# Kernel tuning notes

Measured on AMD Instinct MI355X. Metric: run time of the kernel, lower is better.

The kernel has to match this reference:

```python
import jax, jax.numpy as jnp
import numpy as np

B = 8          # events per batch
NPB = 8192     # points per event (equal counts -> Nmax = NPB)
N = B * NPB
FEAT = 6
K = 128        # max_tokens
TOK = 768      # token_dim
KNN = 16       # k_neighbors
MLP_DIMS = [FEAT, 256, 512, 768, TOK]


def setup_inputs() -> dict:
    key = jax.random.key(0)
    ks = jax.random.split(key, 20)
    coords = jax.random.normal(ks[0], (N, 3), jnp.float32) * 5.0
    features = jax.random.normal(ks[1], (N, FEAT), jnp.float32)
    times = jax.random.uniform(ks[2], (N, 1), jnp.float32)
    # equal-sized, sorted batch ids (8192 points per event)
    batch_ids = jnp.repeat(jnp.arange(B, dtype=jnp.int32), NPB)
    inp = {"coords": coords, "features": features, "batch_ids": batch_ids, "times": times}
    # per-point MLP: 6 -> 256 -> 512 -> 768 -> 768 (last Linear has no ReLU)
    ki = 3
    for i in range(4):
        din, dout = MLP_DIMS[i], MLP_DIMS[i + 1]
        inp[f"W{i+1}"] = jax.random.normal(ks[ki], (din, dout), jnp.float32) / np.sqrt(din); ki += 1
        inp[f"b{i+1}"] = jnp.zeros((dout,), jnp.float32)
    # neighborhood MLP: 768 -> 768 -> 768
    inp["Wn1"] = jax.random.normal(ks[ki], (TOK, TOK), jnp.float32) / np.sqrt(TOK); ki += 1
    inp["bn1"] = jnp.zeros((TOK,), jnp.float32)
    inp["Wn2"] = jax.random.normal(ks[ki], (TOK, TOK), jnp.float32) / np.sqrt(TOK); ki += 1
    inp["bn2"] = jnp.zeros((TOK,), jnp.float32)
    return inp


def _forward(coords, features, batch_ids, times,
             W1, b1, W2, b2, W3, b3, W4, b4, Wn1, bn1, Wn2, bn2):
    INF = jnp.float32(jnp.inf)
    points4 = jnp.concatenate([coords[:, :3], times], axis=-1)  # [N,4] (x,y,z,t)
    # per-point MLP
    h = jax.nn.relu(features @ W1 + b1)
    h = jax.nn.relu(h @ W2 + b2)
    h = jax.nn.relu(h @ W3 + b3)
    feats = h @ W4 + b4                                          # [N,TOK]
    # ---- pack flat -> padded [B, NPB, *] ----
    counts = jnp.bincount(batch_ids, length=B)                   # [B]
    offsets = jnp.cumsum(counts) - counts
    pos = jnp.arange(N) - offsets[batch_ids]
    P = jnp.zeros((B, NPB, 4), points4.dtype).at[batch_ids, pos].set(points4)
    Fp = jnp.zeros((B, NPB, TOK), feats.dtype).at[batch_ids, pos].set(feats)
    valid = jnp.arange(NPB)[None, :] < counts[:, None]           # [B,NPB]
    # ---- small path: take first K points sorted by time ----
    tsort = jnp.where(valid, P[..., 3], INF)
    sorted_idx = jnp.argsort(tsort, axis=1)[:, :K]               # K <= NPB
    tokens_small = jnp.take_along_axis(Fp, sorted_idx[..., None], axis=1)
    cents_small = jnp.take_along_axis(P, sorted_idx[..., None], axis=1)
    masks_small = jnp.arange(K)[None, :] < jnp.minimum(counts, K)[:, None]
    tokens_small = tokens_small * masks_small[..., None]
    cents_small = cents_small * masks_small[..., None]
    # ---- batched FPS over 4D points ----
    min_d0 = jnp.where(valid, INF, 0.0)
    norms = jnp.where(valid, jnp.sum(P * P, axis=-1), -INF)
    first = jnp.argmax(norms, axis=1)                            # farthest-from-origin start
    barange = jnp.arange(B)
    def fps_step(carry, _):
        min_d, last = carry
        c = P[barange, last]                                     # [B,4]
        d = jnp.sum((P - c[:, None, :]) ** 2, axis=-1)
        d = jnp.where(valid, d, INF)
        min_d = jnp.minimum(min_d, d)
        return (min_d, jnp.argmax(min_d, axis=1)), last
    _, idx_seq = jax.lax.scan(fps_step, (min_d0, first), None, length=K)
    fps_idx = idx_seq.T                                          # [B,K]
    validK = jnp.arange(K)[None, :] < jnp.minimum(counts, K)[:, None]
    cents_large = jnp.take_along_axis(P, fps_idx[..., None], axis=1)  # [B,K,4]
    # ---- kNN pooling around centroids ----
    diff = cents_large[:, :, None, :] - P[:, None, :, :]         # [B,K,NPB,4]
    dists = jnp.sum(diff * diff, axis=-1)                        # [B,K,NPB]
    dists = jnp.where(valid[:, None, :], dists, INF)
    k_g = min(KNN, NPB)
    _, knn_idx = jax.lax.top_k(-dists, k_g)                      # smallest-k -> [B,K,k]
    knn_valid = jnp.take_along_axis(jnp.broadcast_to(valid[:, None, :], (B, K, NPB)), knn_idx, axis=2)
    neigh = jnp.take_along_axis(Fp[:, None, :, :], knn_idx[..., None], axis=2)  # [B,K,k,TOK]
    masked = jnp.where(knn_valid[..., None], neigh, -INF)
    pooled = jnp.max(masked, axis=2)
    pooled = jnp.where(jnp.isfinite(pooled), pooled, 0.0)
    tokens_large = jax.nn.relu(pooled @ Wn1 + bn1) @ Wn2 + bn2   # [B,K,TOK]
    # sort selected tokens by centroid time
    ctimes = jnp.where(validK, cents_large[..., 3], INF)
    order = jnp.argsort(ctimes, axis=1)
    tokens_large = jnp.take_along_axis(tokens_large, order[..., None], axis=1)
    cents_large = jnp.take_along_axis(cents_large, order[..., None], axis=1)
    masks_large = jnp.take_along_axis(validK, order, axis=1)
    tokens_large = tokens_large * masks_large[..., None]
    cents_large = cents_large * masks_large[..., None]
    # ---- select per-event path ----
    small = counts <= K
    tokens = jnp.where(small[:, None, None], tokens_small, tokens_large)
    cents = jnp.where(small[:, None, None], cents_small, cents_large)
    masks = jnp.where(small[:, None], masks_small, masks_large)
    return tokens, cents, masks


def reference(coords, features, batch_ids, times,
              W1, b1, W2, b2, W3, b3, W4, b4, Wn1, bn1, Wn2, bn2):
    return _forward(coords, features, batch_ids, times,
                    W1, b1, W2, b2, W3, b3, W4, b4, Wn1, bn1, Wn2, bn2)
```

## Files before the change

kernel.cpp:

```cpp
#include <hip/hip_runtime.h>
#include <hip/hip_bf16.h>


#define BEV 8
#define NPB 8192
#define FEAT 6
#define KTOK 128
#define TOK 768
#define KNN 16

typedef unsigned short ushort_t;
typedef unsigned long long u64;
typedef __bf16 bf16x8 __attribute__((ext_vector_type(8)));
typedef float f32x4 __attribute__((ext_vector_type(4)));
typedef float f32x2 __attribute__((ext_vector_type(2)));

__device__ __forceinline__ ushort_t f2b(float f) {
    union { float f; unsigned int i; } x; x.f = f;
    unsigned int i = x.i;
    unsigned int r = (i + 0x7FFFu + ((i >> 16) & 1u)) >> 16;
    return (ushort_t)r;
}

#define DPP_ROW_SHR1  0x111
#define DPP_ROW_SHR2  0x112
#define DPP_ROW_SHR4  0x114
#define DPP_ROW_SHR8  0x118
#define DPP_ROW_BC15  0x142
#define DPP_ROW_BC31  0x143

template <int CTRL>
__device__ __forceinline__ float dpp_fmax(float v) {
    int o = __builtin_amdgcn_update_dpp(__float_as_int(v), __float_as_int(v),
                                        CTRL, 0xf, 0xf, false);
    return fmaxf(v, __int_as_float(o));
}

template <int CTRL>
__device__ __forceinline__ u64 dpp_u64max(u64 k) {
    int lo = (int)(unsigned)(k & 0xFFFFFFFFu);
    int hi = (int)(unsigned)(k >> 32);
    unsigned olo = (unsigned)__builtin_amdgcn_update_dpp(lo, lo, CTRL, 0xf, 0xf, false);
    unsigned ohi = (unsigned)__builtin_amdgcn_update_dpp(hi, hi, CTRL, 0xf, 0xf, false);
    u64 o = ((u64)ohi << 32) | (u64)olo;
    return o > k ? o : k;
}

__global__ __launch_bounds__(256) void fill_kernel(float* __restrict__ out, int n) {
    int i = blockIdx.x * 256 + threadIdx.x;
    if (i < n) out[i] = 0.f;
}

__global__ __launch_bounds__(1024) void fps_kernel(
    const float* __restrict__ coords, const float* __restrict__ times,
    float* __restrict__ cents, int* __restrict__ pos,
    float* __restrict__ cents_out, float* __restrict__ masks_out)
{
#pragma clang fp contract(off)
    const int b = blockIdx.x;
    const int t = threadIdx.x;
    __shared__ u64   slotk[2][16];
    __shared__ float tarr[KTOK];
    __shared__ float carr[KTOK][4];
    f32x2 px[4], py[4], pz[4], pw[4], md[4];
    const long base = (long)b * NPB;
#pragma unroll
    for (int i = 0; i < 4; ++i) {
        long g = base + t * 8 + i * 2;
        px[i] = (f32x2){coords[g * 3 + 0], coords[(g + 1) * 3 + 0]};
        py[i] = (f32x2){coords[g * 3 + 1], coords[(g + 1) * 3 + 1]};
        pz[i] = (f32x2){coords[g * 3 + 2], coords[(g + 1) * 3 + 2]};
        pw[i] = (f32x2){times[g], times[g + 1]};
        md[i] = (f32x2){__builtin_inff(), __builtin_inff()};
    }
    const int wv = t >> 6, lane = t & 63;
    float cx = 0.f, cy = 0.f, cz = 0.f, cw = 0.f;
    for (int s = 0; s < KTOK; ++s) {
        f32x2 v[4];
        if (s == 0) {
#pragma unroll
            for (int i = 0; i < 4; ++i)
                v[i] = ((px[i]*px[i] + py[i]*py[i]) + pz[i]*pz[i]) + pw[i]*pw[i];
        } else {
            const f32x2 c2x = {cx, cx}, c2y = {cy, cy}, c2z = {cz, cz}, c2w = {cw, cw};
#pragma unroll
            for (int i = 0; i < 4; ++i) {
                f32x2 dx = px[i] - c2x, dy = py[i] - c2y;
                f32x2 dz = pz[i] - c2z, dw = pw[i] - c2w;
                f32x2 d = ((dx*dx + dy*dy) + dz*dz) + dw*dw;
                md[i] = __builtin_elementwise_min(md[i], d);
                v[i] = md[i];
            }
        }
        f32x2 m01 = __builtin_elementwise_max(v[0], v[1]);
        f32x2 m23 = __builtin_elementwise_max(v[2], v[3]);
        f32x2 mm  = __builtin_elementwise_max(m01, m23);
        const float bv = fmaxf(mm[0], mm[1]);
        float mvv = bv;
        mvv = dpp_fmax<DPP_ROW_SHR1>(mvv);
        mvv = dpp_fmax<DPP_ROW_SHR2>(mvv);
        mvv = dpp_fmax<DPP_ROW_SHR4>(mvv);
        mvv = dpp_fmax<DPP_ROW_SHR8>(mvv);
        mvv = dpp_fmax<DPP_ROW_BC15>(mvv);
        mvv = dpp_fmax<DPP_ROW_BC31>(mvv);
        const float mv = __int_as_float(__builtin_amdgcn_readlane(__float_as_int(mvv), 63));
        const u64 mask = __ballot(bv == mv);
        const int wl = __ffsll((long long)mask) - 1;
        const int p = s & 1;
        if (lane == wl) {
            int bi = t * 8;
#pragma unroll
            for (int j = 7; j >= 0; --j)
                if (v[j >> 1][j & 1] == mv) bi = t * 8 + j;
            slotk[p][wv] = ((u64)__float_as_uint(mv) << 32)
                         | (unsigned)(NPB - 1 - bi);
        }
        __syncthreads();
        u64 k1 = slotk[p][lane & 15];
        k1 = dpp_u64max<DPP_ROW_SHR1>(k1);
        k1 = dpp_u64max<DPP_ROW_SHR2>(k1);
        k1 = dpp_u64max<DPP_ROW_SHR4>(k1);
        k1 = dpp_u64max<DPP_ROW_SHR8>(k1);
        const unsigned klo =
            (unsigned)__builtin_amdgcn_readlane((int)(unsigned)(k1 & 0xFFFFFFFFu), 15);
        const int widx = NPB - 1 - (int)klo;
        const long gc = base + widx;
        cx = coords[gc * 3 + 0]; cy = coords[gc * 3 + 1];
        cz = coords[gc * 3 + 2]; cw = times[gc];
        if (t == 0) {
            tarr[s] = cw;
            carr[s][0] = cx; carr[s][1] = cy; carr[s][2] = cz; carr[s][3] = cw;
        }
    }
    __syncthreads();
    if (t < KTOK) {
        const float ti = tarr[t];
        int rank = 0;
        for (int j = 0; j < KTOK; ++j) {
            float tj = tarr[j];
            if (tj < ti || (tj == ti && j < t)) ++rank;
        }
        rank &= (KTOK - 1);
        pos[b * KTOK + t] = rank;
        float* cc = &cents[(b * KTOK + t) * 4];
        cc[0] = carr[t][0]; cc[1] = carr[t][1];
        cc[2] = carr[t][2]; cc[3] = carr[t][3];
#pragma unroll
        for (int c = 0; c < 4; ++c)
            cents_out[(b * KTOK + rank) * 4 + c] = carr[t][c];
        masks_out[b * KTOK + t] = 1.0f;
    }
}

__global__ __launch_bounds__(256) void knn_tc(
    const float* __restrict__ coords, const float* __restrict__ times,
    const float* __restrict__ cents, int* __restrict__ knn_idx,
    const float* __restrict__ W2, ushort_t* __restrict__ Wt2,
    const float* __restrict__ W3, ushort_t* __restrict__ Wt3,
    const float* __restrict__ W4, ushort_t* __restrict__ Wt4)
{
#pragma clang fp contract(off)
    __shared__ float tile[32][33];
    __shared__ float rv[4];
    __shared__ int   ri[4];
    const int blk = blockIdx.x;
    if (blk >= BEV * KTOK) {
        const int id = blk - BEV * KTOK;
        const float* in; ushort_t* out; int K, N, bx, by;
        if (id < 128)      { in = W2; out = Wt2; K = 256; N = 512;
                             bx = id & 15; by = id >> 4; }
        else if (id < 512) { in = W3; out = Wt3; K = 512; N = 768;
                             int r = id - 128; bx = r % 24; by = r / 24; }
        else               { in = W4; out = Wt4; K = 768; N = 768;
                             int r = id - 512; bx = r % 24; by = r / 24; }
        const int tt = threadIdx.x, tx = tt & 31, ty = tt >> 5;
#pragma unroll
        for (int r = 0; r < 4; ++r) {
            int y = by * 32 + ty + r * 8;
            tile[ty + r * 8][tx] = in[(long)y * N + bx * 32 + tx];
        }
        __syncthreads();
        const int ko = by * 32 + tx;
#pragma unroll
        for (int r = 0; r < 4; ++r) {
            int no = bx * 32 + ty + r * 8;
            out[(long)no * K + ko] = f2b(tile[tx][ty + r * 8]);
        }
        return;
    }
    const int b = blk >> 7;
    const int t = threadIdx.x;
    const float cx = cents[blk*4+0], cy = cents[blk*4+1];
    const float cz = cents[blk*4+2], cw = cents[blk*4+3];
    float d[32];
    const long base = (long)b * NPB;
#pragma unroll
    for (int i = 0; i < 32; ++i) {
        long g = base + t * 32 + i;
        float dx = coords[g*3+0] - cx;
        float dy = coords[g*3+1] - cy;
        float dz = coords[g*3+2] - cz;
        float dw = times[g] - cw;
        d[i] = ((dx*dx + dy*dy) + dz*dz) + dw*dw;
    }
    const int wv = t >> 6, lane = t & 63;
    for (int pass = 0; pass < KNN; ++pass) {
        float bvv = __builtin_inff(); int bii = t * 32;
#pragma unroll
        for (int i = 0; i < 32; ++i)
            if (d[i] < bvv) { bvv = d[i]; bii = t * 32 + i; }
        for (int off = 1; off < 64; off <<= 1) {
            float ov = __shfl_xor(bvv, off);
            int   oi = __shfl_xor(bii, off);
            if (ov < bvv || (ov == bvv && oi < bii)) { bvv = ov; bii = oi; }
        }
        if (lane == 0) { rv[wv] = bvv; ri[wv] = bii; }
        __syncthreads();
        float gb = __builtin_inff(); int winner = 0;
        for (int wI = 0; wI < 4; ++wI) {
            float v = rv[wI]; int idx = ri[wI];
            if (v < gb || (v == gb && idx < winner)) { gb = v; winner = idx; }
        }
        winner &= (NPB - 1);
#pragma unroll
        for (int i = 0; i < 32; ++i)
            if (t * 32 + i == winner) d[i] = __builtin_inff();
        if (t == 0) knn_idx[blk * KNN + pass] = winner;
        __syncthreads();
    }
}

#define PAD1 264
#define PAD2 520
#define PAD3 776
__global__ __launch_bounds__(256, 2) void mlp_fused(
    const float* __restrict__ features, const float* __restrict__ W1,
    const float* __restrict__ b1, const int* __restrict__ knn_idx,
    const ushort_t* __restrict__ Wt2, const float* __restrict__ b2,
    const ushort_t* __restrict__ Wt3, const float* __restrict__ b3,
    const ushort_t* __restrict__ Wt4, const float* __restrict__ b4,
    ushort_t* __restrict__ pooled)
{
    __shared__ __align__(16) ushort_t lds[35904];
    ushort_t* h1 = lds;
    ushort_t* h2 = lds + 8448;
    ushort_t* h3 = lds;
    ushort_t* Bs = lds + 25088;
    float*    feat = (float*)(lds + 35328);
    int*      pidx = (int*)(lds + 35840);

    const int bi = blockIdx.x;
    const int t = threadIdx.x;
    const int w = t >> 6, lane = t & 63;
    const int ln = lane & 15, q = lane >> 4;

    if (t < 32) {
        const int c = bi * 2 + (t >> 4);
        const int ev = c >> 7;
        pidx[t] = ev * NPB + (knn_idx[c * KNN + (t & 15)] & (NPB - 1));
    }
    __syncthreads();
    if (t < 192) {
        const int r = t / 6, f = t - r * 6;
        feat[r * 8 + f] = features[(long)pidx[r] * FEAT + f];
    }
    __syncthreads();
    {
        float wv[FEAT];
#pragma unroll
        for (int f = 0; f < FEAT; ++f) wv[f] = W1[f * 256 + t];
        const float bias = b1[t];
#pragma unroll
        for (int r = 0; r < 32; ++r) {
            float acc = 0.f;
#pragma unroll
            for (int f = 0; f < FEAT; ++f) acc += feat[r * 8 + f] * wv[f];
            h1[r * PAD1 + t] = f2b(fmaxf(acc + bias, 0.f));
        }
    }
    __syncthreads();

    {
        f32x4 acc[2][8];
#pragma unroll
        for (int m = 0; m < 2; ++m)
#pragma unroll
            for (int i = 0; i < 8; ++i) acc[m][i] = (f32x4){0,0,0,0};
        for (int k0 = 0; k0 < 256; k0 += 32) {
            bf16x8 af[2];
#pragma unroll
            for (int m = 0; m < 2; ++m)
                af[m] = *(const bf16x8*)(&h1[(m * 16 + ln) * PAD1 + k0 + q * 8]);
#pragma unroll
            for (int np = 0; np < 2; ++np) {
                __syncthreads();
#pragma unroll
                for (int i = 0; i < 4; ++i) {
                    int e = t + i * 256, n = e >> 2, sk = e & 3;
                    *(uint4*)(&Bs[n * 40 + sk * 8]) =
                        *(const uint4*)(Wt2 + (long)(np * 256 + n) * 256 + k0 + sk * 8);
                }
                __syncthreads();
#pragma unroll
                for (int j = 0; j < 4; ++j) {
                    bf16x8 bf = *(const bf16x8*)(&Bs[((w * 4 + j) * 16 + ln) * 40 + q * 8]);
#pragma unroll
                    for (int m = 0; m < 2; ++m)
                        acc[m][np * 4 + j] = __builtin_amdgcn_mfma_f32_16x16x32_bf16(af[m], bf, acc[m][np * 4 + j], 0, 0, 0);
                }
            }
        }
        __syncthreads();
#pragma unroll
        for (int np = 0; np < 2; ++np)
#pragma unroll
            for (int j = 0; j < 4; ++j) {
                const int col = np * 256 + (w * 4 + j) * 16 + ln;
                const float bias = b2[col];
#pragma unroll
                for (int m = 0; m < 2; ++m)
#pragma unroll
                    for (int r = 0; r < 4; ++r)
                        h2[(m * 16 + q * 4 + r) * PAD2 + col] = f2b(fmaxf(acc[m][np * 4 + j][r] + bias, 0.f));
            }
    }
    __syncthreads();

    {
        f32x4 acc[2][12];
#pragma unroll
        for (int m = 0; m < 2; ++m)
#pragma unroll
            for (int i = 0; i < 12; ++i) acc[m][i] = (f32x4){0,0,0,0};
        for (int k0 = 0; k0 < 512; k0 += 32) {
            bf16x8 af[2];
#pragma unroll
            for (int m = 0; m < 2; ++m)
                af[m] = *(const bf16x8*)(&h2[(m * 16 + ln) * PAD2 + k0 + q * 8]);
#pragma unroll
            for (int np = 0; np < 3; ++np) {
                __syncthreads();
#pragma unroll
                for (int i = 0; i < 4; ++i) {
                    int e = t + i * 256, n = e >> 2, sk = e & 3;
                    *(uint4*)(&Bs[n * 40 + sk * 8]) =
                        *(const uint4*)(Wt3 + (long)(np * 256 + n) * 512 + k0 + sk * 8);
                }
                __syncthreads();
#pragma unroll
                for (int j = 0; j < 4; ++j) {
                    bf16x8 bf = *(const bf16x8*)(&Bs[((w * 4 + j) * 16 + ln) * 40 + q * 8]);
#pragma unroll
                    for (int m = 0; m < 2; ++m)
                        acc[m][np * 4 + j] = __builtin_amdgcn_mfma_f32_16x16x32_bf16(af[m], bf, acc[m][np * 4 + j], 0, 0, 0);
                }
            }
        }
        __syncthreads();
#pragma unroll
        for (int np = 0; np < 3; ++np)
#pragma unroll
            for (int j = 0; j < 4; ++j) {
                const int col = np * 256 + (w * 4 + j) * 16 + ln;
                const float bias = b3[col];
#pragma unroll
                for (int m = 0; m < 2; ++m)
#pragma unroll
                    for (int r = 0; r < 4; ++r)
                        h3[(m * 16 + q * 4 + r) * PAD3 + col] = f2b(fmaxf(acc[m][np * 4 + j][r] + bias, 0.f));
            }
    }
    __syncthreads();

    {
        f32x4 acc[2][12];
#pragma unroll
        for (int m = 0; m < 2; ++m)
#pragma unroll
            for (int i = 0; i < 12; ++i) acc[m][i] = (f32x4){0,0,0,0};
        for (int k0 = 0; k0 < 768; k0 += 32) {
            bf16x8 af[2];
#pragma unroll
            for (int m = 0; m < 2; ++m)
                af[m] = *(const bf16x8*)(&h3[(m * 16 + ln) * PAD3 + k0 + q * 8]);
#pragma unroll
            for (int np = 0; np < 3; ++np) {
                __syncthreads();
#pragma unroll
                for (int i = 0; i < 4; ++i) {
                    int e = t + i * 256, n = e >> 2, sk = e & 3;
                    *(uint4*)(&Bs[n * 40 + sk * 8]) =
                        *(const uint4*)(Wt4 + (long)(np * 256 + n) * 768 + k0 + sk * 8);
                }
                __syncthreads();
#pragma unroll
                for (int j = 0; j < 4; ++j) {
                    bf16x8 bf = *(const bf16x8*)(&Bs[((w * 4 + j) * 16 + ln) * 40 + q * 8]);
#pragma unroll
                    for (int m = 0; m < 2; ++m)
                        acc[m][np * 4 + j] = __builtin_amdgcn_mfma_f32_16x16x32_bf16(af[m], bf, acc[m][np * 4 + j], 0, 0, 0);
                }
            }
        }
#pragma unroll
        for (int np = 0; np < 3; ++np)
#pragma unroll
            for (int j = 0; j < 4; ++j) {
                const int col = np * 256 + (w * 4 + j) * 16 + ln;
#pragma unroll
                for (int m = 0; m < 2; ++m) {
                    float v = fmaxf(fmaxf(acc[m][np * 4 + j][0], acc[m][np * 4 + j][1]),
                                    fmaxf(acc[m][np * 4 + j][2], acc[m][np * 4 + j][3]));
                    v = fmaxf(v, __shfl_xor(v, 16));
                    v = fmaxf(v, __shfl_xor(v, 32));
                    if (q == 0)
                        pooled[(long)(bi * 2 + m) * TOK + col] = f2b(v + b4[col]);
                }
            }
    }
}

template<int EPI, int RELU, int F32OUT>
__global__ __launch_bounds__(256) void gemm64_kn(
    const ushort_t* __restrict__ A, const float* __restrict__ B,
    const float* __restrict__ bias, void* __restrict__ Cv,
    int M, int N, int Kd, const int* __restrict__ pos)
{
    __shared__ __align__(16) ushort_t As[64 * 40];
    __shared__ __align__(16) ushort_t Bsh[64 * 40];
    ushort_t* Cb = (ushort_t*)Cv;
    float*    Cf = (float*)Cv;
    const int tid = threadIdx.x;
    const int m0 = blockIdx.x * 64;
    const int n0 = blockIdx.y * 64;
    const int w = tid >> 6, lane = tid & 63;
    const int ln = lane & 15, q = lane >> 4;
    f32x4 acc[4];
#pragma unroll
    for (int ni = 0; ni < 4; ++ni) acc[ni] = (f32x4){0.f, 0.f, 0.f, 0.f};

    const int ar = tid >> 2, as0 = (tid & 3) * 8;
    const int kk = tid >> 4, nn = (tid & 15) * 4;

    for (int k0 = 0; k0 < Kd; k0 += 32) {
        __syncthreads();
        uint4 a0 = *(const uint4*)(A + (long)(m0 + ar) * Kd + k0 + as0);
        float4 f0 = *(const float4*)(B + (long)(k0 + kk)      * N + n0 + nn);
        float4 f1 = *(const float4*)(B + (long)(k0 + kk + 16) * N + n0 + nn);
        *(uint4*)(&As[ar * 40 + as0]) = a0;
        float e0[4] = {f0.x, f0.y, f0.z, f0.w};
        float e1[4] = {f1.x, f1.y, f1.z, f1.w};
#pragma unroll
        for (int j = 0; j < 4; ++j) Bsh[(nn + j) * 40 + kk]      = f2b(e0[j]);
#pragma unroll
        for (int j = 0; j < 4; ++j) Bsh[(nn + j) * 40 + kk + 16] = f2b(e1[j]);
        __syncthreads();
        bf16x8 af = *(const bf16x8*)(&As[(w * 16 + ln) * 40 + q * 8]);
#pragma unroll
        for (int ni = 0; ni < 4; ++ni) {
            bf16x8 bf = *(const bf16x8*)(&Bsh[(ni * 16 + ln) * 40 + q * 8]);
            acc[ni] = __builtin_amdgcn_mfma_f32_16x16x32_bf16(af, bf, acc[ni], 0, 0, 0);
        }
    }

#pragma unroll
    for (int ni = 0; ni < 4; ++ni) {
        const int col = n0 + ni * 16 + ln;
        const float bv = bias[col];
#pragma unroll
        for (int r = 0; r < 4; ++r) {
            const int row = m0 + w * 16 + q * 4 + r;
            float v = acc[ni][r] + bv;
            if (EPI == 0) {
                if (RELU) v = fmaxf(v, 0.f);
                if (F32OUT) Cf[(long)row * N + col] = v;
                else        Cb[(long)row * N + col] = f2b(v);
            } else {
                const int orow = (row & ~(KTOK - 1)) + (pos[row] & (KTOK - 1));
                if (F32OUT) Cf[(long)orow * N + col] = v;
                else        Cb[(long)orow * N + col] = f2b(v);
            }
        }
    }
}

extern "C" void kernel_launch(void* const* d_in, const int* in_sizes, int n_in,
                              void* d_out, int out_size, void* d_ws, size_t ws_size,
                              hipStream_t stream)
{
    const float* coords   = (const float*)d_in[0];
    const float* features = (const float*)d_in[1];
    const float* times    = (const float*)d_in[3];
    const float* W1  = (const float*)d_in[4];
    const float* b1  = (const float*)d_in[5];
    const float* W2  = (const float*)d_in[6];
    const float* b2  = (const float*)d_in[7];
    const float* W3  = (const float*)d_in[8];
    const float* b3  = (const float*)d_in[9];
    const float* W4  = (const float*)d_in[10];
    const float* b4  = (const float*)d_in[11];
    const float* Wn1 = (const float*)d_in[12];
    const float* bn1 = (const float*)d_in[13];
    const float* Wn2 = (const float*)d_in[14];
    const float* bn2 = (const float*)d_in[15];

    char* ws = (char*)d_ws;
    float*    cents   = (float*)(ws + 0);
    int*      pos     = (int*)(ws + 16384);
    int*      knn_idx = (int*)(ws + 20480);
    ushort_t* t1      = (ushort_t*)(ws + 86016);
    ushort_t* pooled  = (ushort_t*)(ws + 1658880);
    ushort_t* Wt2b    = (ushort_t*)(ws + 3231744);
    ushort_t* Wt3b    = (ushort_t*)(ws + 3493888);
    ushort_t* Wt4b    = (ushort_t*)(ws + 4280320);
    const long WS_NEED = 5459968;

    float* tokens_out = (float*)d_out;
    float* cents_out  = tokens_out + 786432;
    float* masks_out  = tokens_out + 790528;

    if ((long)ws_size < WS_NEED) {
        fill_kernel<<<(791552 + 255) / 256, 256, 0, stream>>>(tokens_out, 791552);
        return;
    }

    fps_kernel<<<BEV, 1024, 0, stream>>>(coords, times, cents, pos,
                                         cents_out, masks_out);

    knn_tc<<<BEV * KTOK + 1088, 256, 0, stream>>>(coords, times, cents, knn_idx,
                                                  W2, Wt2b, W3, Wt3b, W4, Wt4b);

    mlp_fused<<<512, 256, 0, stream>>>(features, W1, b1, knn_idx,
                                       Wt2b, b2, Wt3b, b3, Wt4b, b4, pooled);

    gemm64_kn<0,1,0><<<dim3(16, 12), 256, 0, stream>>>(pooled, Wn1, bn1, t1, 1024, 768, 768, nullptr);
    gemm64_kn<2,0,1><<<dim3(16, 12), 256, 0, stream>>>(t1, Wn2, bn2, tokens_out, 1024, 768, 768, pos);
}
```

Measured before the change: 432.7 us.

## Double rows per block and K-step in fused MLP to halve weight traffic

The fused point MLP kernel now handles 4 centroids (64 rows) per 512-thread block instead of 2 centroids per 256-thread block, with two wave groups sharing each staged weight tile. Each staging step loads a 64-wide K slice, so there are half as many barriers and each weight byte is fetched from global memory half as often overall. The cost is that LDS use roughly doubles, to about 140 KB per block, which limits occupancy. Only 256 blocks are launched, fewer than before.

```diff
diff --git a/kernel.cpp b/kernel.cpp
--- a/kernel.cpp
+++ b/kernel.cpp
@@ -233,7 +233,8 @@
 #define PAD1 264
 #define PAD2 520
 #define PAD3 776
-__global__ __launch_bounds__(256, 2) void mlp_fused(
+#define BSP  72
+__global__ __launch_bounds__(512) void mlp_fused(
     const float* __restrict__ features, const float* __restrict__ W1,
     const float* __restrict__ b1, const int* __restrict__ knn_idx,
     const ushort_t* __restrict__ Wt2, const float* __restrict__ b2,
@@ -241,41 +242,45 @@
     const ushort_t* __restrict__ Wt4, const float* __restrict__ b4,
     ushort_t* __restrict__ pooled)
 {
-    __shared__ __align__(16) ushort_t lds[35904];
+    __shared__ __align__(16) ushort_t lds[69760];
     ushort_t* h1 = lds;
-    ushort_t* h2 = lds + 8448;
+    ushort_t* h2 = lds + 16896;
     ushort_t* h3 = lds;
-    ushort_t* Bs = lds + 25088;
-    float*    feat = (float*)(lds + 35328);
-    int*      pidx = (int*)(lds + 35840);
+    ushort_t* Bs = lds + 50176;
+    float*    feat = (float*)(lds + 68608);
+    int*      pidx = (int*)(lds + 69632);
 
     const int bi = blockIdx.x;
     const int t = threadIdx.x;
     const int w = t >> 6, lane = t & 63;
     const int ln = lane & 15, q = lane >> 4;
-
-    if (t < 32) {
-        const int c = bi * 2 + (t >> 4);
+    const int mg = w >> 2;
+    const int wn = w & 3;
+
+    if (t < 64) {
+        const int c = bi * 4 + (t >> 4);
         const int ev = c >> 7;
         pidx[t] = ev * NPB + (knn_idx[c * KNN + (t & 15)] & (NPB - 1));
     }
     __syncthreads();
-    if (t < 192) {
+    if (t < 384) {
         const int r = t / 6, f = t - r * 6;
         feat[r * 8 + f] = features[(long)pidx[r] * FEAT + f];
     }
     __syncthreads();
     {
+        const int col = t & 255, half = t >> 8;
         float wv[FEAT];
 #pragma unroll
-        for (int f = 0; f < FEAT; ++f) wv[f] = W1[f * 256 + t];
-        const float bias = b1[t];
+        for (int f = 0; f < FEAT; ++f) wv[f] = W1[f * 256 + col];
+        const float bias = b1[col];
 #pragma unroll
         for (int r = 0; r < 32; ++r) {
+            const int row = half * 32 + r;
             float acc = 0.f;
 #pragma unroll
-            for (int f = 0; f < FEAT; ++f) acc += feat[r * 8 + f] * wv[f];
-            h1[r * PAD1 + t] = f2b(fmaxf(acc + bias, 0.f));
+            for (int f = 0; f < FEAT; ++f) acc += feat[row * 8 + f] * wv[f];
+            h1[row * PAD1 + col] = f2b(fmaxf(acc + bias, 0.f));
         }
     }
     __syncthreads();
@@ -286,27 +291,33 @@
         for (int m = 0; m < 2; ++m)
 #pragma unroll
             for (int i = 0; i < 8; ++i) acc[m][i] = (f32x4){0,0,0,0};
-        for (int k0 = 0; k0 < 256; k0 += 32) {
-            bf16x8 af[2];
+        for (int k0 = 0; k0 < 256; k0 += 64) {
+            bf16x8 af[2][2];
 #pragma unroll
             for (int m = 0; m < 2; ++m)
-                af[m] = *(const bf16x8*)(&h1[(m * 16 + ln) * PAD1 + k0 + q * 8]);
+#pragma unroll
+                for (int kh = 0; kh < 2; ++kh)
+                    af[m][kh] = *(const bf16x8*)(&h1[(mg * 32 + m * 16 + ln) * PAD1 + k0 + kh * 32 + q * 8]);
 #pragma unroll
             for (int np = 0; np < 2; ++np) {
                 __syncthreads();
 #pragma unroll
                 for (int i = 0; i < 4; ++i) {
-                    int e = t + i * 256, n = e >> 2, sk = e & 3;
-                    *(uint4*)(&Bs[n * 40 + sk * 8]) =
+                    int e = t + i * 512, n = e >> 3, sk = e & 7;
+                    *(uint4*)(&Bs[n * BSP + sk * 8]) =
                         *(const uint4*)(Wt2 + (long)(np * 256 + n) * 256 + k0 + sk * 8);
                 }
                 __syncthreads();
 #pragma unroll
                 for (int j = 0; j < 4; ++j) {
-                    bf16x8 bf = *(const bf16x8*)(&Bs[((w * 4 + j) * 16 + ln) * 40 + q * 8]);
-#pragma unroll
-                    for (int m = 0; m < 2; ++m)
-                        acc[m][np * 4 + j] = __builtin_amdgcn_mfma_f32_16x16x32_bf16(af[m], bf, acc[m][np * 4 + j], 0, 0, 0);
+                    const int row = (wn * 4 + j) * 16 + ln;
+                    bf16x8 bf0 = *(const bf16x8*)(&Bs[row * BSP + q * 8]);
+                    bf16x8 bf1 = *(const bf16x8*)(&Bs[row * BSP + 32 + q * 8]);
+#pragma unroll
+                    for (int m = 0; m < 2; ++m) {
+                        acc[m][np * 4 + j] = __builtin_amdgcn_mfma_f32_16x16x32_bf16(af[m][0], bf0, acc[m][np * 4 + j], 0, 0, 0);
+                        acc[m][np * 4 + j] = __builtin_amdgcn_mfma_f32_16x16x32_bf16(af[m][1], bf1, acc[m][np * 4 + j], 0, 0, 0);
+                    }
                 }
             }
         }
@@ -315,13 +326,13 @@
         for (int np = 0; np < 2; ++np)
 #pragma unroll
             for (int j = 0; j < 4; ++j) {
-                const int col = np * 256 + (w * 4 + j) * 16 + ln;
+                const int col = np * 256 + (wn * 4 + j) * 16 + ln;
                 const float bias = b2[col];
 #pragma unroll
                 for (int m = 0; m < 2; ++m)
 #pragma unroll
                     for (int r = 0; r < 4; ++r)
-                        h2[(m * 16 + q * 4 + r) * PAD2 + col] = f2b(fmaxf(acc[m][np * 4 + j][r] + bias, 0.f));
+                        h2[(mg * 32 + m * 16 + q * 4 + r) * PAD2 + col] = f2b(fmaxf(acc[m][np * 4 + j][r] + bias, 0.f));
             }
     }
     __syncthreads();
@@ -332,27 +343,33 @@
         for (int m = 0; m < 2; ++m)
 #pragma unroll
             for (int i = 0; i < 12; ++i) acc[m][i] = (f32x4){0,0,0,0};
-        for (int k0 = 0; k0 < 512; k0 += 32) {
-            bf16x8 af[2];
+        for (int k0 = 0; k0 < 512; k0 += 64) {
+            bf16x8 af[2][2];
 #pragma unroll
             for (int m = 0; m < 2; ++m)
-                af[m] = *(const bf16x8*)(&h2[(m * 16 + ln) * PAD2 + k0 + q * 8]);
+#pragma unroll
+                for (int kh = 0; kh < 2; ++kh)
+                    af[m][kh] = *(const bf16x8*)(&h2[(mg * 32 + m * 16 + ln) * PAD2 + k0 + kh * 32 + q * 8]);
 #pragma unroll
             for (int np = 0; np < 3; ++np) {
                 __syncthreads();
 #pragma unroll
                 for (int i = 0; i < 4; ++i) {
-                    int e = t + i * 256, n = e >> 2, sk = e & 3;
-                    *(uint4*)(&Bs[n * 40 + sk * 8]) =
+                    int e = t + i * 512, n = e >> 3, sk = e & 7;
+                    *(uint4*)(&Bs[n * BSP + sk * 8]) =
                         *(const uint4*)(Wt3 + (long)(np * 256 + n) * 512 + k0 + sk * 8);
                 }
                 __syncthreads();
 #pragma unroll
                 for (int j = 0; j < 4; ++j) {
-                    bf16x8 bf = *(const bf16x8*)(&Bs[((w * 4 + j) * 16 + ln) * 40 + q * 8]);
-#pragma unroll
-                    for (int m = 0; m < 2; ++m)
-                        acc[m][np * 4 + j] = __builtin_amdgcn_mfma_f32_16x16x32_bf16(af[m], bf, acc[m][np * 4 + j], 0, 0, 0);
+                    const int row = (wn * 4 + j) * 16 + ln;
+                    bf16x8 bf0 = *(const bf16x8*)(&Bs[row * BSP + q * 8]);
+                    bf16x8 bf1 = *(const bf16x8*)(&Bs[row * BSP + 32 + q * 8]);
+#pragma unroll
+                    for (int m = 0; m < 2; ++m) {
+                        acc[m][np * 4 + j] = __builtin_amdgcn_mfma_f32_16x16x32_bf16(af[m][0], bf0, acc[m][np * 4 + j], 0, 0, 0);
+                        acc[m][np * 4 + j] = __builtin_amdgcn_mfma_f32_16x16x32_bf16(af[m][1], bf1, acc[m][np * 4 + j], 0, 0, 0);
+                    }
                 }
             }
         }
@@ -361,13 +378,13 @@
         for (int np = 0; np < 3; ++np)
 #pragma unroll
             for (int j = 0; j < 4; ++j) {
-                const int col = np * 256 + (w * 4 + j) * 16 + ln;
+                const int col = np * 256 + (wn * 4 + j) * 16 + ln;
                 const float bias = b3[col];
 #pragma unroll
                 for (int m = 0; m < 2; ++m)
 #pragma unroll
                     for (int r = 0; r < 4; ++r)
-                        h3[(m * 16 + q * 4 + r) * PAD3 + col] = f2b(fmaxf(acc[m][np * 4 + j][r] + bias, 0.f));
+                        h3[(mg * 32 + m * 16 + q * 4 + r) * PAD3 + col] = f2b(fmaxf(acc[m][np * 4 + j][r] + bias, 0.f));
             }
     }
     __syncthreads();
@@ -378,27 +395,33 @@
         for (int m = 0; m < 2; ++m)
 #pragma unroll
             for (int i = 0; i < 12; ++i) acc[m][i] = (f32x4){0,0,0,0};
-        for (int k0 = 0; k0 < 768; k0 += 32) {
-            bf16x8 af[2];
+        for (int k0 = 0; k0 < 768; k0 += 64) {
+            bf16x8 af[2][2];
 #pragma unroll
             for (int m = 0; m < 2; ++m)
-                af[m] = *(const bf16x8*)(&h3[(m * 16 + ln) * PAD3 + k0 + q * 8]);
+#pragma unroll
+                for (int kh = 0; kh < 2; ++kh)
+                    af[m][kh] = *(const bf16x8*)(&h3[(mg * 32 + m * 16 + ln) * PAD3 + k0 + kh * 32 + q * 8]);
 #pragma unroll
             for (int np = 0; np < 3; ++np) {
                 __syncthreads();
 #pragma unroll
                 for (int i = 0; i < 4; ++i) {
-                    int e = t + i * 256, n = e >> 2, sk = e & 3;
-                    *(uint4*)(&Bs[n * 40 + sk * 8]) =
+                    int e = t + i * 512, n = e >> 3, sk = e & 7;
+                    *(uint4*)(&Bs[n * BSP + sk * 8]) =
                         *(const uint4*)(Wt4 + (long)(np * 256 + n) * 768 + k0 + sk * 8);
                 }
                 __syncthreads();
 #pragma unroll
                 for (int j = 0; j < 4; ++j) {
-                    bf16x8 bf = *(const bf16x8*)(&Bs[((w * 4 + j) * 16 + ln) * 40 + q * 8]);
-#pragma unroll
-                    for (int m = 0; m < 2; ++m)
-                        acc[m][np * 4 + j] = __builtin_amdgcn_mfma_f32_16x16x32_bf16(af[m], bf, acc[m][np * 4 + j], 0, 0, 0);
+                    const int row = (wn * 4 + j) * 16 + ln;
+                    bf16x8 bf0 = *(const bf16x8*)(&Bs[row * BSP + q * 8]);
+                    bf16x8 bf1 = *(const bf16x8*)(&Bs[row * BSP + 32 + q * 8]);
+#pragma unroll
+                    for (int m = 0; m < 2; ++m) {
+                        acc[m][np * 4 + j] = __builtin_amdgcn_mfma_f32_16x16x32_bf16(af[m][0], bf0, acc[m][np * 4 + j], 0, 0, 0);
+                        acc[m][np * 4 + j] = __builtin_amdgcn_mfma_f32_16x16x32_bf16(af[m][1], bf1, acc[m][np * 4 + j], 0, 0, 0);
+                    }
                 }
             }
         }
@@ -406,7 +429,7 @@
         for (int np = 0; np < 3; ++np)
 #pragma unroll
             for (int j = 0; j < 4; ++j) {
-                const int col = np * 256 + (w * 4 + j) * 16 + ln;
+                const int col = np * 256 + (wn * 4 + j) * 16 + ln;
 #pragma unroll
                 for (int m = 0; m < 2; ++m) {
                     float v = fmaxf(fmaxf(acc[m][np * 4 + j][0], acc[m][np * 4 + j][1]),
@@ -414,7 +437,7 @@
                     v = fmaxf(v, __shfl_xor(v, 16));
                     v = fmaxf(v, __shfl_xor(v, 32));
                     if (q == 0)
-                        pooled[(long)(bi * 2 + m) * TOK + col] = f2b(v + b4[col]);
+                        pooled[(long)(bi * 4 + mg * 2 + m) * TOK + col] = f2b(v + b4[col]);
                 }
             }
     }
@@ -530,7 +553,7 @@
     knn_tc<<<BEV * KTOK + 1088, 256, 0, stream>>>(coords, times, cents, knn_idx,
                                                   W2, Wt2b, W3, Wt3b, W4, Wt4b);
 
-    mlp_fused<<<512, 256, 0, stream>>>(features, W1, b1, knn_idx,
+    mlp_fused<<<256, 512, 0, stream>>>(features, W1, b1, knn_idx,
                                        Wt2b, b2, Wt3b, b3, Wt4b, b4, pooled);
 
     gemm64_kn<0,1,0><<<dim3(16, 12), 256, 0, stream>>>(pooled, Wn1, bn1, t1, 1024, 768, 768, nullptr);
```

Result: faster. 413.7 us (-4.4%).
